# Kernel optimization log

Measured on AMD Instinct MI355X. Metric: run time of the kernel, lower is better.

Reference implementation:

```python
import jax, jax.numpy as jnp
import numpy as np

EPS = 0.1   # module __init__ default eps
TAU = 1.0   # map_em default tau


def _mog_eval(pi, mu, Sigma, data):
    # pi: (B,p), mu/Sigma: (B,p,d), data: (B,N,d)
    d = data.shape[-1]
    inv_S = 1.0 / Sigma
    jll = -0.5 * (
        d * jnp.log(2.0 * jnp.pi)
        + jnp.log(Sigma).sum(-1)[:, None, :]                      # (B,1,p)
        + jnp.einsum('bnd,bpd->bnp', data * data, inv_S)          # Mahalanobis x^2 term
        + (mu * mu * inv_S).sum(-1)[:, None, :]                   # mu^2/Sigma term
        - 2.0 * jnp.einsum('bnd,bpd->bnp', data, mu * inv_S)      # cross term
    ) + jnp.log(pi)[:, None, :]
    mll = jax.nn.logsumexp(jll, axis=-1)          # (B,N)
    cll = jll - mll[..., None]                    # (B,N,p)
    return jll, cll, mll


def _map_m_step(data, weight, m, V, tau):
    # data: (B,N,d), weight: (B,N,p), m/V: (p,d)
    wsum = weight.sum(1)                                  # (B,p)
    wsum_reg = wsum + tau
    wxsum = jnp.einsum('bnp,bnd->bpd', weight, data)
    wxxsum = jnp.einsum('bnp,bnd->bpd', weight, data * data)
    pi = wsum_reg / wsum_reg.sum(1, keepdims=True)
    mu = (wxsum + m[None] * tau) / wsum_reg[..., None]
    Sigma = (wxxsum + (V + m * m)[None] * tau) / wsum_reg[..., None] - mu * mu
    return pi, mu, Sigma


def setup_inputs() -> dict:
    key = jax.random.key(0)
    k1, k2 = jax.random.split(key)
    B, N, d, p = 8, 4096, 1024, 16
    data = jax.random.normal(k1, (B, N, d), dtype=jnp.float32)
    mask = jnp.ones((B, N), dtype=jnp.float32)
    m = 0.1 * jax.random.normal(k2, (p, d), dtype=jnp.float32)
    V_ = jnp.full((p, d), np.log(np.e - 1.0), dtype=jnp.float32)
    return {"data": data, "mask": mask, "m": m, "V_": V_, "num_iters": 3}


def reference(data, mask, m, V_, num_iters):
    B, N, d = data.shape
    p = m.shape[0]
    # prior (DirNIWNet.forward + mode)
    V = EPS * jax.nn.softplus(V_)
    pi = jnp.full((B, p), 1.0 / p, dtype=data.dtype)
    mu = jnp.broadcast_to(m, (B, p, d)).astype(data.dtype)
    Sigma = jnp.broadcast_to(V, (B, p, d)).astype(data.dtype)
    qq = jnp.zeros((B, N, p), dtype=data.dtype)
    for _ in range(num_iters):  # small fixed iteration count (EM)
        _, cll, _ = _mog_eval(pi, mu, Sigma, data)
        qq = jnp.exp(cll) * mask[..., None]
        pi, mu, Sigma = _map_m_step(data, qq, m, V, TAU)
    return pi, mu, Sigma, qq
```

## Files before the change

kernel.cpp:

```cpp
#include <hip/hip_runtime.h>
#include <math.h>

#define BB 8
#define NN 4096
#define DD 1024
#define PP 16
#define KS 8
#define KC (DD / KS)

static constexpr float DLOG2PI = 1881.9861160031696f;
static constexpr float EPSC = 0.1f;


__global__ __launch_bounds__(256) void k_init(const float* __restrict__ m,
                                              const float* __restrict__ V_,
                                              float* __restrict__ Wmat,
                                              float* __restrict__ cns)
{
    int j = blockIdx.x, b = blockIdx.y;
    int tid = threadIdx.x;
    __shared__ float red[512];
    int d0 = tid * 4;
    float4 m4 = *(const float4*)(m + j * DD + d0);
    float4 v4 = *(const float4*)(V_ + j * DD + d0);
    float mv[4] = {m4.x, m4.y, m4.z, m4.w};
    float vv[4] = {v4.x, v4.y, v4.z, v4.w};
    float* Wb = Wmat + (size_t)b * (DD * 32);
    float llog = 0.f, lmq = 0.f;
#pragma unroll
    for (int c = 0; c < 4; c++) {
        float V = EPSC * log1pf(expf(vv[c]));
        float inv = 1.0f / V;
        int d = d0 + c;
        Wb[d * 32 + j * 2] = inv;
        Wb[d * 32 + j * 2 + 1] = mv[c] * inv;
        llog += logf(V);
        lmq += mv[c] * mv[c] * inv;
    }
    red[tid] = llog; red[256 + tid] = lmq;
    __syncthreads();
    for (int s = 128; s > 0; s >>= 1) {
        if (tid < s) { red[tid] += red[tid + s]; red[256 + tid] += red[256 + tid + s]; }
        __syncthreads();
    }
    if (tid == 0)
        cns[b * PP + j] = logf(1.0f / 16.0f) - 0.5f * (DLOG2PI + red[0] + red[256]);
}

__global__ __launch_bounds__(256) void k_estep(const float* __restrict__ X,
                                               const float* __restrict__ Wmat,
                                               float* __restrict__ epart)
{
    int rb = blockIdx.x, ks = blockIdx.y, b = blockIdx.z;
    int tid = threadIdx.x;
    int n = rb * 256 + tid;
    const float* xp = X + ((size_t)b * NN + n) * DD + ks * KC;
    const float* wp = Wmat + (size_t)b * (DD * 32) + (size_t)(ks * KC) * 32;
    float acc1[16] = {0,0,0,0,0,0,0,0,0,0,0,0,0,0,0,0};
    float acc2[16] = {0,0,0,0,0,0,0,0,0,0,0,0,0,0,0,0};
#pragma unroll 1
    for (int kk = 0; kk < KC; kk += 16) {
        float4 xv[4];
#pragma unroll
        for (int u = 0; u < 4; u++) xv[u] = *(const float4*)(xp + kk + u * 4);
        const float* w = wp + (size_t)kk * 32;
#pragma unroll
        for (int u = 0; u < 4; u++) {
            float xs[4] = {xv[u].x, xv[u].y, xv[u].z, xv[u].w};
#pragma unroll
            for (int c = 0; c < 4; c++) {
                float xvv = xs[c];
                float xq = xvv * xvv;
                const float* wk = w + (u * 4 + c) * 32;
#pragma unroll
                for (int j = 0; j < 16; j++) {
                    acc1[j] = fmaf(xq,  wk[2 * j],     acc1[j]);
                    acc2[j] = fmaf(xvv, wk[2 * j + 1], acc2[j]);
                }
            }
        }
    }
    float* ep = epart + (((size_t)ks * BB + b) * NN + n) * PP;
#pragma unroll
    for (int q = 0; q < 4; q++) {
        float4 v = make_float4(-0.5f * acc1[q * 4 + 0] + acc2[q * 4 + 0],
                               -0.5f * acc1[q * 4 + 1] + acc2[q * 4 + 1],
                               -0.5f * acc1[q * 4 + 2] + acc2[q * 4 + 2],
                               -0.5f * acc1[q * 4 + 3] + acc2[q * 4 + 3]);
        *(float4*)(ep + q * 4) = v;
    }
}

__global__ __launch_bounds__(128) void k_ereduce(const float* __restrict__ epart,
                                                 const float* __restrict__ mask,
                                                 const float* __restrict__ cns,
                                                 float* __restrict__ qq)
{
    int chunk = blockIdx.x, b = blockIdx.y;
    int tid = threadIdx.x;
    int n = chunk * 128 + tid;
    __shared__ float cs[16];
    if (tid < 16) cs[tid] = cns[b * PP + tid];
    __syncthreads();
    float jl[16];
#pragma unroll
    for (int q = 0; q < 4; q++) {
        float4 v = *(const float4*)(epart + ((size_t)b * NN + n) * PP + q * 4);
        jl[q * 4 + 0] = v.x; jl[q * 4 + 1] = v.y; jl[q * 4 + 2] = v.z; jl[q * 4 + 3] = v.w;
    }
#pragma unroll
    for (int ks = 1; ks < KS; ks++) {
#pragma unroll
        for (int q = 0; q < 4; q++) {
            float4 v = *(const float4*)(epart + (((size_t)ks * BB + b) * NN + n) * PP + q * 4);
            jl[q * 4 + 0] += v.x; jl[q * 4 + 1] += v.y; jl[q * 4 + 2] += v.z; jl[q * 4 + 3] += v.w;
        }
    }
    float mx = -3.4e38f;
#pragma unroll
    for (int j = 0; j < 16; j++) { jl[j] += cs[j]; mx = fmaxf(mx, jl[j]); }
    float sum = 0.f;
#pragma unroll
    for (int j = 0; j < 16; j++) { jl[j] = expf(jl[j] - mx); sum += jl[j]; }
    float r = mask[(size_t)b * NN + n] / sum;
    float* qo = qq + ((size_t)b * NN + n) * PP;
#pragma unroll
    for (int q = 0; q < 4; q++)
        *(float4*)(qo + q * 4) = make_float4(jl[q * 4 + 0] * r, jl[q * 4 + 1] * r,
                                             jl[q * 4 + 2] * r, jl[q * 4 + 3] * r);
}

__global__ __launch_bounds__(512) void k_mstep(const float* __restrict__ X,
                                               const float* __restrict__ qq,
                                               float* __restrict__ wxp,
                                               float* __restrict__ wxxp)
{
    int nq = blockIdx.x, b = blockIdx.y;
    int tid = threadIdx.x;
    int cg = tid & 255;
    int ph = tid >> 8;
    int col0 = cg * 4;
    const float* Xb = X + (size_t)b * NN * DD;
    const float* qb = qq + (size_t)b * NN * PP;
    float aw[16][4] = {};
    float ax[16][4] = {};
#pragma unroll 2
    for (int i = 0; i < 64; i++) {
        int n = nq * 128 + i * 2 + ph;
        float4 x = *(const float4*)(Xb + (size_t)n * DD + col0);
        const float* q = qb + (size_t)n * PP;
        float x2x = x.x * x.x, x2y = x.y * x.y, x2z = x.z * x.z, x2w = x.w * x.w;
#pragma unroll
        for (int j = 0; j < 16; j++) {
            float qj = q[j];
            aw[j][0] = fmaf(qj, x.x, aw[j][0]);
            aw[j][1] = fmaf(qj, x.y, aw[j][1]);
            aw[j][2] = fmaf(qj, x.z, aw[j][2]);
            aw[j][3] = fmaf(qj, x.w, aw[j][3]);
            ax[j][0] = fmaf(qj, x2x, ax[j][0]);
            ax[j][1] = fmaf(qj, x2y, ax[j][1]);
            ax[j][2] = fmaf(qj, x2z, ax[j][2]);
            ax[j][3] = fmaf(qj, x2w, ax[j][3]);
        }
    }
    __shared__ float red[256 * 33];
#define MSTEP_PASS(SRC, JB, DST)                                               \
    __syncthreads();                                                           \
    if (ph == 1) {                                                             \
        _Pragma("unroll")                                                      \
        for (int jj = 0; jj < 8; jj++)                                         \
            *(float4*)(&red[cg * 33 + jj * 4]) =                               \
                make_float4(SRC[(JB) + jj][0], SRC[(JB) + jj][1],              \
                            SRC[(JB) + jj][2], SRC[(JB) + jj][3]);             \
    }                                                                          \
    __syncthreads();                                                           \
    if (ph == 0) {                                                             \
        _Pragma("unroll")                                                      \
        for (int jj = 0; jj < 8; jj++) {                                       \
            float4 o = *(float4*)(&red[cg * 33 + jj * 4]);                     \
            o.x += SRC[(JB) + jj][0];                                          \
            o.y += SRC[(JB) + jj][1];                                          \
            o.z += SRC[(JB) + jj][2];                                          \
            o.w += SRC[(JB) + jj][3];                                          \
            *(float4*)(DST + (((size_t)b * 32 + nq) * PP + (JB) + jj) * DD +   \
                       col0) = o;                                              \
        }                                                                      \
    }
    MSTEP_PASS(aw, 0, wxp)
    MSTEP_PASS(aw, 8, wxp)
    MSTEP_PASS(ax, 0, wxxp)
    MSTEP_PASS(ax, 8, wxxp)
#undef MSTEP_PASS
}

__global__ __launch_bounds__(256) void k_finalize(const float* __restrict__ qq,
                                                  const float* __restrict__ wxp,
                                                  const float* __restrict__ wxxp,
                                                  const float* __restrict__ m,
                                                  const float* __restrict__ V_,
                                                  float* __restrict__ pi,
                                                  float* __restrict__ mu,
                                                  float* __restrict__ Sigma,
                                                  float* __restrict__ Wmat,
                                                  float* __restrict__ cns)
{
    int j = blockIdx.x, b = blockIdx.y;
    int tid = threadIdx.x;
    __shared__ float red[256 * 17 + 8];
    __shared__ float wsr[16];
    __shared__ float sden;
    const float* qb = qq + (size_t)b * NN * PP;
    float ws[16] = {0,0,0,0,0,0,0,0,0,0,0,0,0,0,0,0};
    for (int i = 0; i < 16; i++) {
        int n = tid + i * 256;
        const float4 q0 = *(const float4*)(qb + (size_t)n * PP + 0);
        const float4 q1 = *(const float4*)(qb + (size_t)n * PP + 4);
        const float4 q2 = *(const float4*)(qb + (size_t)n * PP + 8);
        const float4 q3 = *(const float4*)(qb + (size_t)n * PP + 12);
        ws[0] += q0.x; ws[1] += q0.y; ws[2] += q0.z; ws[3] += q0.w;
        ws[4] += q1.x; ws[5] += q1.y; ws[6] += q1.z; ws[7] += q1.w;
        ws[8] += q2.x; ws[9] += q2.y; ws[10] += q2.z; ws[11] += q2.w;
        ws[12] += q3.x; ws[13] += q3.y; ws[14] += q3.z; ws[15] += q3.w;
    }
#pragma unroll
    for (int jj = 0; jj < 16; jj++) red[tid * 17 + jj] = ws[jj];
    __syncthreads();
    if (tid < 16) {
        float s = 0.f;
        for (int t = 0; t < 256; t++) s += red[t * 17 + tid];
        wsr[tid] = s + 1.0f;
    }
    __syncthreads();
    if (tid == 0) {
        float dd = 0.f;
#pragma unroll
        for (int jj = 0; jj < 16; jj++) dd += wsr[jj];
        sden = dd;
    }
    __syncthreads();
    float rws = 1.0f / wsr[j];
    float pij = wsr[j] / sden;
    int d0 = tid * 4;
    float wxa[4] = {0, 0, 0, 0}, wxxa[4] = {0, 0, 0, 0};
#pragma unroll
    for (int g = 0; g < 32; g++) {
        const float4 a = *(const float4*)(wxp + (((size_t)b * 32 + g) * PP + j) * DD + d0);
        wxa[0] += a.x; wxa[1] += a.y; wxa[2] += a.z; wxa[3] += a.w;
        const float4 c2 = *(const float4*)(wxxp + (((size_t)b * 32 + g) * PP + j) * DD + d0);
        wxxa[0] += c2.x; wxxa[1] += c2.y; wxxa[2] += c2.z; wxxa[3] += c2.w;
    }
    float4 m4 = *(const float4*)(m + j * DD + d0);
    float4 v4 = *(const float4*)(V_ + j * DD + d0);
    float mvv[4] = {m4.x, m4.y, m4.z, m4.w};
    float vvv[4] = {v4.x, v4.y, v4.z, v4.w};
    float muo[4], sgo[4];
    float llog = 0.f, lmq = 0.f;
    float* Wb = Wmat + (size_t)b * (DD * 32);
#pragma unroll
    for (int c = 0; c < 4; c++) {
        float V = EPSC * log1pf(expf(vvv[c]));
        float muv = (wxa[c] + mvv[c]) * rws;
        float Sg = (wxxa[c] + V + mvv[c] * mvv[c]) * rws - muv * muv;
        float inv = 1.0f / Sg;
        muo[c] = muv; sgo[c] = Sg;
        int d = d0 + c;
        Wb[d * 32 + j * 2] = inv;
        Wb[d * 32 + j * 2 + 1] = muv * inv;
        llog += logf(Sg);
        lmq += muv * muv * inv;
    }
    *(float4*)(mu + ((size_t)b * PP + j) * DD + d0) = make_float4(muo[0], muo[1], muo[2], muo[3]);
    *(float4*)(Sigma + ((size_t)b * PP + j) * DD + d0) = make_float4(sgo[0], sgo[1], sgo[2], sgo[3]);
    red[tid] = llog; red[4096 + tid] = lmq;
    __syncthreads();
    for (int s = 128; s > 0; s >>= 1) {
        if (tid < s) { red[tid] += red[tid + s]; red[4096 + tid] += red[4096 + tid + s]; }
        __syncthreads();
    }
    if (tid == 0) {
        pi[b * PP + j] = pij;
        cns[b * PP + j] = logf(pij) - 0.5f * (DLOG2PI + red[0] + red[4096]);
    }
}

extern "C" void kernel_launch(void* const* d_in, const int* in_sizes, int n_in,
                              void* d_out, int out_size, void* d_ws, size_t ws_size,
                              hipStream_t stream)
{
    (void)in_sizes; (void)n_in; (void)out_size; (void)ws_size;
    const float* data = (const float*)d_in[0];
    const float* mask = (const float*)d_in[1];
    const float* m    = (const float*)d_in[2];
    const float* V_   = (const float*)d_in[3];

    float* out = (float*)d_out;
    float* pi  = out;
    float* mu  = out + 128;
    float* Sg  = out + 128 + 131072;
    float* qq  = out + 128 + 2 * 131072;

    float* ws    = (float*)d_ws;
    float* Wmat  = ws;
    float* cns   = ws + 262144;
    float* epart = ws + 262272;
    float* wxp   = ws + 262272 + 4194304;
    float* wxxp  = ws + 262272 + 2 * 4194304;

    k_init<<<dim3(16, 8), 256, 0, stream>>>(m, V_, Wmat, cns);
    for (int it = 0; it < 3; it++) {
        k_estep<<<dim3(16, KS, 8), 256, 0, stream>>>(data, Wmat, epart);
        k_ereduce<<<dim3(32, 8), 128, 0, stream>>>(epart, mask, cns, qq);
        k_mstep<<<dim3(32, 8), 512, 0, stream>>>(data, qq, wxp, wxxp);
        k_finalize<<<dim3(16, 8), 256, 0, stream>>>(qq, wxp, wxxp, m, V_, pi, mu, Sg, Wmat, cns);
    }
}
```

Measured before the change: 513.7 us.

## Double-buffer X loads in E/M steps, two rows per thread, fuse weight sums

The E-step kernel now handles two data rows per thread, so each weight read is reused twice, and it software-pipelines its float4 loads of X across 16-column tiles. The M-step loop double-buffers the X row load ahead of the FMA block. Per-component weight sums are now computed as partial sums inside the E-step reduce kernel, so the finalize kernel no longer rescans the full qq array. The costs are more registers (possible lower occupancy), half as many E-step blocks, and an extra workspace buffer.

```diff
diff --git a/kernel.cpp b/kernel.cpp
--- a/kernel.cpp
+++ b/kernel.cpp
@@ -11,6 +11,8 @@
 static constexpr float DLOG2PI = 1881.9861160031696f;
 static constexpr float EPSC = 0.1f;
 
+
+#define FELEM(v, c) ((c) == 0 ? (v).x : (c) == 1 ? (v).y : (c) == 2 ? (v).z : (v).w)
 
 __global__ __launch_bounds__(256) void k_init(const float* __restrict__ m,
                                               const float* __restrict__ V_,
@@ -53,53 +55,76 @@
 {
     int rb = blockIdx.x, ks = blockIdx.y, b = blockIdx.z;
     int tid = threadIdx.x;
-    int n = rb * 256 + tid;
-    const float* xp = X + ((size_t)b * NN + n) * DD + ks * KC;
+    int n0 = rb * 512 + tid * 2;
+    const float* xp0 = X + ((size_t)b * NN + n0) * DD + ks * KC;
+    const float* xp1 = xp0 + DD;
     const float* wp = Wmat + (size_t)b * (DD * 32) + (size_t)(ks * KC) * 32;
-    float acc1[16] = {0,0,0,0,0,0,0,0,0,0,0,0,0,0,0,0};
-    float acc2[16] = {0,0,0,0,0,0,0,0,0,0,0,0,0,0,0,0};
+    float a1[2][16] = {};
+    float a2[2][16] = {};
+    float4 cur[8], nxt[8];
+
+#define ESTEP_LOAD(BUF, T)                                                     \
+    _Pragma("unroll")                                                          \
+    for (int u = 0; u < 4; u++) {                                              \
+        BUF[u]     = *(const float4*)(xp0 + (T) * 16 + u * 4);                 \
+        BUF[4 + u] = *(const float4*)(xp1 + (T) * 16 + u * 4);                 \
+    }
+
+#define ESTEP_COMPUTE(BUF, T)                                                  \
+    _Pragma("unroll")                                                          \
+    for (int u = 0; u < 4; u++) {                                              \
+        _Pragma("unroll")                                                      \
+        for (int c = 0; c < 4; c++) {                                          \
+            const float* wk = wp + ((T) * 16 + u * 4 + c) * 32;                \
+            float xv0 = FELEM(BUF[u], c),     xq0 = xv0 * xv0;                 \
+            float xv1 = FELEM(BUF[4 + u], c), xq1 = xv1 * xv1;                 \
+            _Pragma("unroll")                                                  \
+            for (int j = 0; j < 16; j++) {                                     \
+                a1[0][j] = fmaf(xq0, wk[2 * j],     a1[0][j]);                 \
+                a2[0][j] = fmaf(xv0, wk[2 * j + 1], a2[0][j]);                 \
+                a1[1][j] = fmaf(xq1, wk[2 * j],     a1[1][j]);                 \
+                a2[1][j] = fmaf(xv1, wk[2 * j + 1], a2[1][j]);                 \
+            }                                                                  \
+        }                                                                      \
+    }
+
+    ESTEP_LOAD(cur, 0)
 #pragma unroll 1
-    for (int kk = 0; kk < KC; kk += 16) {
-        float4 xv[4];
-#pragma unroll
-        for (int u = 0; u < 4; u++) xv[u] = *(const float4*)(xp + kk + u * 4);
-        const float* w = wp + (size_t)kk * 32;
-#pragma unroll
-        for (int u = 0; u < 4; u++) {
-            float xs[4] = {xv[u].x, xv[u].y, xv[u].z, xv[u].w};
-#pragma unroll
-            for (int c = 0; c < 4; c++) {
-                float xvv = xs[c];
-                float xq = xvv * xvv;
-                const float* wk = w + (u * 4 + c) * 32;
-#pragma unroll
-                for (int j = 0; j < 16; j++) {
-                    acc1[j] = fmaf(xq,  wk[2 * j],     acc1[j]);
-                    acc2[j] = fmaf(xvv, wk[2 * j + 1], acc2[j]);
-                }
-            }
+    for (int t = 0; t < 8; t += 2) {
+        ESTEP_LOAD(nxt, t + 1)
+        ESTEP_COMPUTE(cur, t)
+        int t2 = (t + 2 < 8) ? t + 2 : 0;
+        ESTEP_LOAD(cur, t2)
+        ESTEP_COMPUTE(nxt, t + 1)
+    }
+#undef ESTEP_LOAD
+#undef ESTEP_COMPUTE
+
+    float* ep = epart + (((size_t)ks * BB + b) * NN + n0) * PP;
+#pragma unroll
+    for (int r = 0; r < 2; r++) {
+#pragma unroll
+        for (int q = 0; q < 4; q++) {
+            float4 v = make_float4(-0.5f * a1[r][q * 4 + 0] + a2[r][q * 4 + 0],
+                                   -0.5f * a1[r][q * 4 + 1] + a2[r][q * 4 + 1],
+                                   -0.5f * a1[r][q * 4 + 2] + a2[r][q * 4 + 2],
+                                   -0.5f * a1[r][q * 4 + 3] + a2[r][q * 4 + 3]);
+            *(float4*)(ep + r * PP + q * 4) = v;
         }
-    }
-    float* ep = epart + (((size_t)ks * BB + b) * NN + n) * PP;
-#pragma unroll
-    for (int q = 0; q < 4; q++) {
-        float4 v = make_float4(-0.5f * acc1[q * 4 + 0] + acc2[q * 4 + 0],
-                               -0.5f * acc1[q * 4 + 1] + acc2[q * 4 + 1],
-                               -0.5f * acc1[q * 4 + 2] + acc2[q * 4 + 2],
-                               -0.5f * acc1[q * 4 + 3] + acc2[q * 4 + 3]);
-        *(float4*)(ep + q * 4) = v;
     }
 }
 
 __global__ __launch_bounds__(128) void k_ereduce(const float* __restrict__ epart,
                                                  const float* __restrict__ mask,
                                                  const float* __restrict__ cns,
-                                                 float* __restrict__ qq)
+                                                 float* __restrict__ qq,
+                                                 float* __restrict__ wsum_p)
 {
     int chunk = blockIdx.x, b = blockIdx.y;
     int tid = threadIdx.x;
     int n = chunk * 128 + tid;
     __shared__ float cs[16];
+    __shared__ float red[128 * 17];
     if (tid < 16) cs[tid] = cns[b * PP + tid];
     __syncthreads();
     float jl[16];
@@ -125,9 +150,22 @@
     float r = mask[(size_t)b * NN + n] / sum;
     float* qo = qq + ((size_t)b * NN + n) * PP;
 #pragma unroll
-    for (int q = 0; q < 4; q++)
-        *(float4*)(qo + q * 4) = make_float4(jl[q * 4 + 0] * r, jl[q * 4 + 1] * r,
-                                             jl[q * 4 + 2] * r, jl[q * 4 + 3] * r);
+    for (int q = 0; q < 4; q++) {
+        float4 v = make_float4(jl[q * 4 + 0] * r, jl[q * 4 + 1] * r,
+                               jl[q * 4 + 2] * r, jl[q * 4 + 3] * r);
+        *(float4*)(qo + q * 4) = v;
+        red[tid * 17 + q * 4 + 0] = v.x;
+        red[tid * 17 + q * 4 + 1] = v.y;
+        red[tid * 17 + q * 4 + 2] = v.z;
+        red[tid * 17 + q * 4 + 3] = v.w;
+    }
+    __syncthreads();
+    if (tid < 16) {
+        float s = 0.f;
+#pragma unroll 8
+        for (int t = 0; t < 128; t++) s += red[t * 17 + tid];
+        wsum_p[((size_t)b * 32 + chunk) * 16 + tid] = s;
+    }
 }
 
 __global__ __launch_bounds__(512) void k_mstep(const float* __restrict__ X,
@@ -142,27 +180,43 @@
     int col0 = cg * 4;
     const float* Xb = X + (size_t)b * NN * DD;
     const float* qb = qq + (size_t)b * NN * PP;
+    int nbase = nq * 128 + ph;
     float aw[16][4] = {};
     float ax[16][4] = {};
-#pragma unroll 2
-    for (int i = 0; i < 64; i++) {
-        int n = nq * 128 + i * 2 + ph;
-        float4 x = *(const float4*)(Xb + (size_t)n * DD + col0);
-        const float* q = qb + (size_t)n * PP;
-        float x2x = x.x * x.x, x2y = x.y * x.y, x2z = x.z * x.z, x2w = x.w * x.w;
-#pragma unroll
-        for (int j = 0; j < 16; j++) {
-            float qj = q[j];
-            aw[j][0] = fmaf(qj, x.x, aw[j][0]);
-            aw[j][1] = fmaf(qj, x.y, aw[j][1]);
-            aw[j][2] = fmaf(qj, x.z, aw[j][2]);
-            aw[j][3] = fmaf(qj, x.w, aw[j][3]);
-            ax[j][0] = fmaf(qj, x2x, ax[j][0]);
-            ax[j][1] = fmaf(qj, x2y, ax[j][1]);
-            ax[j][2] = fmaf(qj, x2z, ax[j][2]);
-            ax[j][3] = fmaf(qj, x2w, ax[j][3]);
-        }
-    }
+
+#define MSTEP_FMA(XV, QP)                                                      \
+    {                                                                          \
+        float x2x = (XV).x * (XV).x, x2y = (XV).y * (XV).y;                    \
+        float x2z = (XV).z * (XV).z, x2w = (XV).w * (XV).w;                    \
+        _Pragma("unroll")                                                      \
+        for (int j = 0; j < 16; j++) {                                         \
+            float qj = (QP)[j];                                                \
+            aw[j][0] = fmaf(qj, (XV).x, aw[j][0]);                             \
+            aw[j][1] = fmaf(qj, (XV).y, aw[j][1]);                             \
+            aw[j][2] = fmaf(qj, (XV).z, aw[j][2]);                             \
+            aw[j][3] = fmaf(qj, (XV).w, aw[j][3]);                             \
+            ax[j][0] = fmaf(qj, x2x, ax[j][0]);                                \
+            ax[j][1] = fmaf(qj, x2y, ax[j][1]);                                \
+            ax[j][2] = fmaf(qj, x2z, ax[j][2]);                                \
+            ax[j][3] = fmaf(qj, x2w, ax[j][3]);                                \
+        }                                                                      \
+    }
+
+    float4 xc = *(const float4*)(Xb + (size_t)nbase * DD + col0);
+#pragma unroll 1
+    for (int i = 0; i < 64; i += 2) {
+        int na = nbase + i * 2;
+        int nb_ = nbase + (i + 1) * 2;
+        float4 xn = *(const float4*)(Xb + (size_t)nb_ * DD + col0);
+        const float* q0 = qb + (size_t)na * PP;
+        MSTEP_FMA(xc, q0)
+        int i2 = (i + 2 < 64) ? i + 2 : 0;
+        xc = *(const float4*)(Xb + (size_t)(nbase + i2 * 2) * DD + col0);
+        const float* q1 = qb + (size_t)nb_ * PP;
+        MSTEP_FMA(xn, q1)
+    }
+#undef MSTEP_FMA
+
     __shared__ float red[256 * 33];
 #define MSTEP_PASS(SRC, JB, DST)                                               \
     __syncthreads();                                                           \
@@ -193,7 +247,7 @@
 #undef MSTEP_PASS
 }
 
-__global__ __launch_bounds__(256) void k_finalize(const float* __restrict__ qq,
+__global__ __launch_bounds__(256) void k_finalize(const float* __restrict__ wsum_p,
                                                   const float* __restrict__ wxp,
                                                   const float* __restrict__ wxxp,
                                                   const float* __restrict__ m,
@@ -206,28 +260,21 @@
 {
     int j = blockIdx.x, b = blockIdx.y;
     int tid = threadIdx.x;
-    __shared__ float red[256 * 17 + 8];
+    __shared__ float red[512];
+    __shared__ float redw[16 * 17];
     __shared__ float wsr[16];
     __shared__ float sden;
-    const float* qb = qq + (size_t)b * NN * PP;
-    float ws[16] = {0,0,0,0,0,0,0,0,0,0,0,0,0,0,0,0};
-    for (int i = 0; i < 16; i++) {
-        int n = tid + i * 256;
-        const float4 q0 = *(const float4*)(qb + (size_t)n * PP + 0);
-        const float4 q1 = *(const float4*)(qb + (size_t)n * PP + 4);
-        const float4 q2 = *(const float4*)(qb + (size_t)n * PP + 8);
-        const float4 q3 = *(const float4*)(qb + (size_t)n * PP + 12);
-        ws[0] += q0.x; ws[1] += q0.y; ws[2] += q0.z; ws[3] += q0.w;
-        ws[4] += q1.x; ws[5] += q1.y; ws[6] += q1.z; ws[7] += q1.w;
-        ws[8] += q2.x; ws[9] += q2.y; ws[10] += q2.z; ws[11] += q2.w;
-        ws[12] += q3.x; ws[13] += q3.y; ws[14] += q3.z; ws[15] += q3.w;
-    }
-#pragma unroll
-    for (int jj = 0; jj < 16; jj++) red[tid * 17 + jj] = ws[jj];
+    {
+        int j2 = tid & 15, c2 = tid >> 4;
+        float s = wsum_p[((size_t)b * 32 + 2 * c2) * 16 + j2]
+                + wsum_p[((size_t)b * 32 + 2 * c2 + 1) * 16 + j2];
+        redw[c2 * 17 + j2] = s;
+    }
     __syncthreads();
     if (tid < 16) {
         float s = 0.f;
-        for (int t = 0; t < 256; t++) s += red[t * 17 + tid];
+#pragma unroll
+        for (int c2 = 0; c2 < 16; c2++) s += redw[c2 * 17 + tid];
         wsr[tid] = s + 1.0f;
     }
     __syncthreads();
@@ -271,15 +318,15 @@
     }
     *(float4*)(mu + ((size_t)b * PP + j) * DD + d0) = make_float4(muo[0], muo[1], muo[2], muo[3]);
     *(float4*)(Sigma + ((size_t)b * PP + j) * DD + d0) = make_float4(sgo[0], sgo[1], sgo[2], sgo[3]);
-    red[tid] = llog; red[4096 + tid] = lmq;
+    red[tid] = llog; red[256 + tid] = lmq;
     __syncthreads();
     for (int s = 128; s > 0; s >>= 1) {
-        if (tid < s) { red[tid] += red[tid + s]; red[4096 + tid] += red[4096 + tid + s]; }
+        if (tid < s) { red[tid] += red[tid + s]; red[256 + tid] += red[256 + tid + s]; }
         __syncthreads();
     }
     if (tid == 0) {
         pi[b * PP + j] = pij;
-        cns[b * PP + j] = logf(pij) - 0.5f * (DLOG2PI + red[0] + red[4096]);
+        cns[b * PP + j] = logf(pij) - 0.5f * (DLOG2PI + red[0] + red[256]);
     }
 }
 
@@ -299,18 +346,19 @@
     float* Sg  = out + 128 + 131072;
     float* qq  = out + 128 + 2 * 131072;
 
-    float* ws    = (float*)d_ws;
-    float* Wmat  = ws;
-    float* cns   = ws + 262144;
-    float* epart = ws + 262272;
-    float* wxp   = ws + 262272 + 4194304;
-    float* wxxp  = ws + 262272 + 2 * 4194304;
+    float* ws     = (float*)d_ws;
+    float* Wmat   = ws;
+    float* cns    = ws + 262144;
+    float* epart  = ws + 262272;
+    float* wxp    = ws + 262272 + 4194304;
+    float* wxxp   = ws + 262272 + 2 * 4194304;
+    float* wsum_p = ws + 262272 + 3 * 4194304;
 
     k_init<<<dim3(16, 8), 256, 0, stream>>>(m, V_, Wmat, cns);
     for (int it = 0; it < 3; it++) {
-        k_estep<<<dim3(16, KS, 8), 256, 0, stream>>>(data, Wmat, epart);
-        k_ereduce<<<dim3(32, 8), 128, 0, stream>>>(epart, mask, cns, qq);
+        k_estep<<<dim3(8, KS, 8), 256, 0, stream>>>(data, Wmat, epart);
+        k_ereduce<<<dim3(32, 8), 128, 0, stream>>>(epart, mask, cns, qq, wsum_p);
         k_mstep<<<dim3(32, 8), 512, 0, stream>>>(data, qq, wxp, wxxp);
-        k_finalize<<<dim3(16, 8), 256, 0, stream>>>(qq, wxp, wxxp, m, V_, pi, mu, Sg, Wmat, cns);
-    }
-}
+        k_finalize<<<dim3(16, 8), 256, 0, stream>>>(wsum_p, wxp, wxxp, m, V_, pi, mu, Sg, Wmat, cns);
+    }
+}
```

Result: no change. 510.9 us (-0.6%).
